# Performance work log

Hardware: AMD Instinct MI355X
Metric: run time of the kernel (lower is better)

Reference implementation:

```python
import jax, jax.numpy as jnp
import numpy as np

N = 100000
IN_CH = 128
HID = 128
H = HID // 2  # per-sign half width = 64
E = 1200000
L = 3  # num_layers


def _mean_agg(x, src, dst, n):
    # mean of x[src] scattered to dst (source_to_target message passing)
    s = jax.ops.segment_sum(x[src], dst, num_segments=n)
    cnt = jax.ops.segment_sum(jnp.ones(src.shape[0], x.dtype), dst, num_segments=n)
    return s / jnp.maximum(cnt, 1.0)[:, None]


def setup_inputs() -> dict:
    key = jax.random.key(0)
    ks = jax.random.split(key, 16)
    sc = 0.05
    inp = {
        "x": jax.random.normal(ks[0], (N, IN_CH), jnp.float32),
        "pos_edge_index": jax.random.randint(ks[1], (2, E), 0, N, jnp.int64),
        "neg_edge_index": jax.random.randint(ks[2], (2, E), 0, N, jnp.int64),
        # conv1 (first_aggr=True): per-sign Linear on aggregated + on root
        "Wp_l": jax.random.normal(ks[3], (IN_CH, H), jnp.float32) * sc,
        "Wp_r": jax.random.normal(ks[4], (IN_CH, H), jnp.float32) * sc,
        "bp": jnp.zeros((H,), jnp.float32),
        "Wn_l": jax.random.normal(ks[5], (IN_CH, H), jnp.float32) * sc,
        "Wn_r": jax.random.normal(ks[6], (IN_CH, H), jnp.float32) * sc,
        "bn": jnp.zeros((H,), jnp.float32),
        # convs (first_aggr=False), stacked over L-1 layers
        "Wl_pos": jax.random.normal(ks[7], (L - 1, 2 * H, H), jnp.float32) * sc,
        "Wr_pos": jax.random.normal(ks[8], (L - 1, H, H), jnp.float32) * sc,
        "b_pos": jnp.zeros((L - 1, H), jnp.float32),
        "Wl_neg": jax.random.normal(ks[9], (L - 1, 2 * H, H), jnp.float32) * sc,
        "Wr_neg": jax.random.normal(ks[10], (L - 1, H, H), jnp.float32) * sc,
        "b_neg": jnp.zeros((L - 1, H), jnp.float32),
    }
    return inp


def reference(x, pos_edge_index, neg_edge_index,
              Wp_l, Wp_r, bp, Wn_l, Wn_r, bn,
              Wl_pos, Wr_pos, b_pos, Wl_neg, Wr_neg, b_neg):
    n = x.shape[0]
    ps, pd = pos_edge_index[0], pos_edge_index[1]
    ns, nd = neg_edge_index[0], neg_edge_index[1]

    # ---- conv1, first_aggr=True ----
    agg_p = _mean_agg(x, ps, pd, n)   # [N, IN_CH]
    agg_n = _mean_agg(x, ns, nd, n)
    out_pos = agg_p @ Wp_l + x @ Wp_r + bp   # [N, H]
    out_neg = agg_n @ Wn_l + x @ Wn_r + bn
    z = jnp.tanh(jnp.concatenate([out_pos, out_neg], axis=1))  # [N, 2H]

    # ---- convs, first_aggr=False ----
    for l in range(Wl_pos.shape[0]):
        x_p, x_n = z[:, :H], z[:, H:]
        ap_p = _mean_agg(x_p, ps, pd, n)   # pos-agg of pos half
        an_n = _mean_agg(x_n, ns, nd, n)   # neg-agg of neg half
        ap_n = _mean_agg(x_n, ps, pd, n)   # pos-agg of neg half
        an_p = _mean_agg(x_p, ns, nd, n)   # neg-agg of pos half
        o_p = (jnp.concatenate([ap_p, an_n], axis=1) @ Wl_pos[l]
               + x_p @ Wr_pos[l] + b_pos[l])
        o_n = (jnp.concatenate([ap_n, an_p], axis=1) @ Wl_neg[l]
               + x_n @ Wr_neg[l] + b_neg[l])
        z = jnp.tanh(jnp.concatenate([o_p, o_n], axis=1))
    return z  # [N, HID]
```

## Files before the change

kernel.cpp:

```cpp
#include <hip/hip_runtime.h>
#include <math.h>

#define CH 128
#define BSHIFT 9
#define BNODES (1 << BSHIFT)
#define CHUNKE 16384

typedef __attribute__((ext_vector_type(8))) short bf16x8;
typedef __attribute__((ext_vector_type(4))) float f32x4;

__global__ __launch_bounds__(256) void hist_kernel(const int* __restrict__ pe,
                                                   const int* __restrict__ ne,
                                                   int* __restrict__ hb,
                                                   int NBr, int G, int M, int E) {
    const int g = blockIdx.x, s = blockIdx.y, t = threadIdx.x;
    const int* __restrict__ dst = (s ? ne : pe) + E;
    __shared__ int h[512];
    for (int i = t; i < NBr; i += 256) h[i] = 0;
    __syncthreads();
    const int e0 = g * CHUNKE, e1 = min(e0 + CHUNKE, E);
    for (int e = e0 + t; e < e1; e += 256) atomicAdd(&h[dst[e] >> BSHIFT], 1);
    __syncthreads();
    int* out = hb + (size_t)s * M;
    for (int b = t; b < NBr; b += 256) out[b * G + g] = h[b];
}

__global__ __launch_bounds__(1024) void hscan_kernel(int* __restrict__ hb, int M) {
    const int s = blockIdx.y, t = threadIdx.x;
    int* H = hb + (size_t)s * M;
    const int K = (M + 1023) >> 10;
    const int i0 = t * K, i1 = min(i0 + K, M);
    int sum = 0;
    for (int i = i0; i < i1; ++i) sum += H[i];
    __shared__ int sh[1024];
    sh[t] = sum;
    __syncthreads();
    for (int off = 1; off < 1024; off <<= 1) {
        int v = (t >= off) ? sh[t - off] : 0;
        __syncthreads();
        sh[t] += v;
        __syncthreads();
    }
    int run = sh[t] - sum;
    for (int i = i0; i < i1; ++i) { int v = H[i]; H[i] = run; run += v; }
}

__global__ __launch_bounds__(256) void scatter_kernel(const int* __restrict__ pe,
                                                      const int* __restrict__ ne,
                                                      const int* __restrict__ hb,
                                                      int* __restrict__ tmp,
                                                      int NBr, int G, int M, int E) {
    const int g = blockIdx.x, s = blockIdx.y, t = threadIdx.x;
    const int* __restrict__ ed = s ? ne : pe;
    const int* off = hb + (size_t)s * M;
    __shared__ int cur[512];
    for (int b = t; b < NBr; b += 256) cur[b] = off[b * G + g];
    __syncthreads();
    int* out = tmp + (size_t)s * E;
    const int e0 = g * CHUNKE, e1 = min(e0 + CHUNKE, E);
    for (int e = e0 + t; e < e1; e += 256) {
        const int src = ed[e], d = ed[E + e];
        const int p = atomicAdd(&cur[d >> BSHIFT], 1);
        out[p] = (src << BSHIFT) | (d & (BNODES - 1));
    }
}

__global__ __launch_bounds__(256) void bucket_kernel(const int* __restrict__ tmp,
                                                     const int* __restrict__ hb,
                                                     int* __restrict__ row_p,
                                                     int* __restrict__ row_n,
                                                     int* __restrict__ csr_p,
                                                     int* __restrict__ csr_n,
                                                     int NBr, int G, int M, int E, int nN) {
    const int b = blockIdx.x, s = blockIdx.y, t = threadIdx.x;
    const int* off = hb + (size_t)s * M;
    const int lo = off[b * G];
    const int hi = (b + 1 < NBr) ? off[(b + 1) * G] : E;
    const int base = b << BSHIFT;
    const int nloc = min(BNODES, nN - base);
    const int* __restrict__ in = tmp + (size_t)s * E;
    int* __restrict__ row = s ? row_n : row_p;
    int* __restrict__ csr = s ? csr_n : csr_p;
    __shared__ int cnt[BNODES];
    __shared__ int psum[256];
    for (int i = t; i < BNODES; i += 256) cnt[i] = 0;
    __syncthreads();
    for (int e = lo + t; e < hi; e += 256) atomicAdd(&cnt[in[e] & (BNODES - 1)], 1);
    __syncthreads();
    const int c0 = cnt[2 * t], c1 = cnt[2 * t + 1];
    const int ps = c0 + c1;
    psum[t] = ps;
    __syncthreads();
    for (int o = 1; o < 256; o <<= 1) {
        int v = (t >= o) ? psum[t - o] : 0;
        __syncthreads();
        psum[t] += v;
        __syncthreads();
    }
    const int ex = psum[t] - ps;
    cnt[2 * t]     = lo + ex;
    cnt[2 * t + 1] = lo + ex + c0;
    if (2 * t < nloc)     row[base + 2 * t] = lo + ex;
    if (2 * t + 1 < nloc) row[base + 2 * t + 1] = lo + ex + c0;
    if (b == NBr - 1 && t == 0) row[nN] = E;
    __syncthreads();
    for (int e = lo + t; e < hi; e += 256) {
        const int v = in[e];
        const int p = atomicAdd(&cnt[v & (BNODES - 1)], 1);
        csr[p] = (v >> BSHIFT) << 8;
    }
}

__device__ __forceinline__ float fast_tanh(float x) {
    float e = __expf(2.0f * x);
    return 1.0f - 2.0f * __builtin_amdgcn_rcpf(e + 1.0f);
}

__device__ __forceinline__ unsigned short f2bf(float f) {
    unsigned u = __float_as_uint(f);
    u += 0x7fffu + ((u >> 16) & 1u);
    return (unsigned short)(u >> 16);
}

__device__ __forceinline__ float bf_lo(unsigned v) { return __uint_as_float(v << 16); }
__device__ __forceinline__ float bf_hi(unsigned v) { return __uint_as_float(v & 0xffff0000u); }

__global__ __launch_bounds__(256) void cvt_kernel(const float* __restrict__ x,
                                                  unsigned short* __restrict__ xb,
                                                  int total8) {
    const int i = blockIdx.x * 256 + threadIdx.x;
    if (i >= total8) return;
    const float4 u0 = ((const float4*)x)[2 * i];
    const float4 u1 = ((const float4*)x)[2 * i + 1];
    union { bf16x8 v; unsigned short u[8]; } o;
    o.u[0] = f2bf(u0.x); o.u[1] = f2bf(u0.y); o.u[2] = f2bf(u0.z); o.u[3] = f2bf(u0.w);
    o.u[4] = f2bf(u1.x); o.u[5] = f2bf(u1.y); o.u[6] = f2bf(u1.z); o.u[7] = f2bf(u1.w);
    ((bf16x8*)xb)[i] = o.v;
}

#define P1(csr, e, A0, A1, A2, A3) { \
    const int o0 = csr[e], o1 = csr[e + 1]; \
    const uint2 w = *(const uint2*)(fB + (half ? o1 : o0) + off8); \
    A0 += bf_lo(w.x); A1 += bf_hi(w.x); A2 += bf_lo(w.y); A3 += bf_hi(w.y); }

#define T1(csr, e, A0, A1, A2, A3) { \
    if (half == 0) { \
        const uint2 w = *(const uint2*)(fB + csr[e] + off8); \
        A0 += bf_lo(w.x); A1 += bf_hi(w.x); A2 += bf_lo(w.y); A3 += bf_hi(w.y); } }

__global__ __launch_bounds__(256) void agg_kernel(
    const unsigned short* __restrict__ feat,
    unsigned* __restrict__ aggp, unsigned* __restrict__ aggn,
    const int* __restrict__ row_p, const int* __restrict__ csr_p,
    const int* __restrict__ row_n, const int* __restrict__ csr_n, int nN) {
    const int t = threadIdx.x;
    const int wave = t >> 6;
    const int lane = t & 63;
    const int node = blockIdx.x * 4 + wave;
    if (node >= nN) return;
    const char* __restrict__ fB = (const char*)feat;
    const int half = lane >> 5;
    const int off8 = (lane & 31) * 8;
    int ep = __builtin_amdgcn_readfirstlane(row_p[node]);
    const int e1p = __builtin_amdgcn_readfirstlane(row_p[node + 1]);
    int en = __builtin_amdgcn_readfirstlane(row_n[node]);
    const int e1n = __builtin_amdgcn_readfirstlane(row_n[node + 1]);
    const int degp = e1p - ep;
    const int degn = e1n - en;
    float p0 = 0.f, p1 = 0.f, p2 = 0.f, p3 = 0.f;
    float n0 = 0.f, n1 = 0.f, n2 = 0.f, n3 = 0.f;
    while (ep + 8 <= e1p && en + 8 <= e1n) {
        P1(csr_p, ep,     p0, p1, p2, p3);
        P1(csr_p, ep + 2, p0, p1, p2, p3);
        P1(csr_p, ep + 4, p0, p1, p2, p3);
        P1(csr_p, ep + 6, p0, p1, p2, p3);
        P1(csr_n, en,     n0, n1, n2, n3);
        P1(csr_n, en + 2, n0, n1, n2, n3);
        P1(csr_n, en + 4, n0, n1, n2, n3);
        P1(csr_n, en + 6, n0, n1, n2, n3);
        ep += 8; en += 8;
    }
    while (ep + 2 <= e1p && en + 2 <= e1n) {
        P1(csr_p, ep, p0, p1, p2, p3);
        P1(csr_n, en, n0, n1, n2, n3);
        ep += 2; en += 2;
    }
    for (; ep + 1 < e1p; ep += 2) P1(csr_p, ep, p0, p1, p2, p3);
    if (ep < e1p) T1(csr_p, ep, p0, p1, p2, p3);
    for (; en + 1 < e1n; en += 2) P1(csr_n, en, n0, n1, n2, n3);
    if (en < e1n) T1(csr_n, en, n0, n1, n2, n3);

    p0 += __shfl_xor(p0, 32); p1 += __shfl_xor(p1, 32);
    p2 += __shfl_xor(p2, 32); p3 += __shfl_xor(p3, 32);
    n0 += __shfl_xor(n0, 32); n1 += __shfl_xor(n1, 32);
    n2 += __shfl_xor(n2, 32); n3 += __shfl_xor(n3, 32);

    const float invp = 1.0f / (float)(degp > 1 ? degp : 1);
    const float invn = 1.0f / (float)(degn > 1 ? degn : 1);
    const int li = lane & 31;
    if (half == 0) {
        uint2 o;
        o.x = (unsigned)f2bf(p0 * invp) | ((unsigned)f2bf(p1 * invp) << 16);
        o.y = (unsigned)f2bf(p2 * invp) | ((unsigned)f2bf(p3 * invp) << 16);
        ((uint2*)(aggp + (size_t)node * 64))[li] = o;
    } else {
        uint2 o;
        o.x = (unsigned)f2bf(n0 * invn) | ((unsigned)f2bf(n1 * invn) << 16);
        o.y = (unsigned)f2bf(n2 * invn) | ((unsigned)f2bf(n3 * invn) << 16);
        ((uint2*)(aggn + (size_t)node * 64))[li] = o;
    }
}

__global__ __launch_bounds__(64) void wpack_kernel(
    const float* __restrict__ Wp_l, const float* __restrict__ Wp_r,
    const float* __restrict__ Wn_l, const float* __restrict__ Wn_r,
    const float* __restrict__ Wl_pos, const float* __restrict__ Wr_pos,
    const float* __restrict__ Wl_neg, const float* __restrict__ Wr_neg,
    unsigned short* __restrict__ Wpk) {
    const int b = blockIdx.x;
    const int L = b / 96;
    const int rem = b % 96;
    const int ks = rem / 8, nt = rem % 8;
    const int lane = threadIdx.x;
    const int kb = ks * 32 + (lane >> 4) * 8;
    const int n = nt * 16 + (lane & 15);
    unsigned short v[8];
#pragma unroll
    for (int j = 0; j < 8; ++j) {
        const int k = kb + j;
        float w = 0.f;
        if (L == 0) {
            if (k < 128)      w = (n < 64) ? Wp_l[k * 64 + n] : 0.f;
            else if (k < 256) w = (n < 64) ? 0.f : Wn_l[(k - 128) * 64 + (n - 64)];
            else              w = (n < 64) ? Wp_r[(k - 256) * 64 + n]
                                           : Wn_r[(k - 256) * 64 + (n - 64)];
        } else {
            const float* WLp = Wl_pos + (size_t)(L - 1) * 128 * 64;
            const float* WLn = Wl_neg + (size_t)(L - 1) * 128 * 64;
            const float* WRp = Wr_pos + (size_t)(L - 1) * 64 * 64;
            const float* WRn = Wr_neg + (size_t)(L - 1) * 64 * 64;
            if (k < 64)       w = (n < 64) ? WLp[k * 64 + n] : 0.f;
            else if (k < 128) w = (n < 64) ? 0.f : WLn[(k - 64) * 64 + (n - 64)];
            else if (k < 192) w = (n < 64) ? 0.f : WLn[(64 + k - 128) * 64 + (n - 64)];
            else if (k < 256) w = (n < 64) ? WLp[(64 + k - 192) * 64 + n] : 0.f;
            else if (k < 320) w = (n < 64) ? WRp[(k - 256) * 64 + n] : 0.f;
            else              w = (n < 64) ? 0.f : WRn[(k - 320) * 64 + (n - 64)];
        }
        v[j] = f2bf(w);
    }
    unsigned short* dst = Wpk + (size_t)b * 512 + lane * 8;
#pragma unroll
    for (int j = 0; j < 8; ++j) dst[j] = v[j];
}

__global__ void bcat_kernel(const float* __restrict__ bp, const float* __restrict__ bn,
                            const float* __restrict__ b_pos, const float* __restrict__ b_neg,
                            float* __restrict__ bcat) {
    int t = threadIdx.x;
    int L = t >> 7, n = t & 127;
    float v;
    if (L == 0) v = (n < 64) ? bp[n] : bn[n - 64];
    else        v = (n < 64) ? b_pos[(L - 1) * 64 + n] : b_neg[(L - 1) * 64 + (n - 64)];
    bcat[t] = v;
}

template <bool OUTF32>
__global__ __launch_bounds__(256) void gemm_kernel(
    const unsigned short* __restrict__ aggp, const unsigned short* __restrict__ aggn,
    const unsigned short* __restrict__ feat, const unsigned short* __restrict__ Wpk,
    const float* __restrict__ bcat, void* __restrict__ outv, int nN) {
    const int t = threadIdx.x;
    const int wave = __builtin_amdgcn_readfirstlane(t >> 6);
    const int lane = t & 63;
    const int r0 = blockIdx.x * 64 + wave * 16;
    int rowA = r0 + (lane & 15);
    if (rowA >= nN) rowA = nN - 1;
    const int koff = (lane >> 4) * 8;

    __shared__ unsigned short wlds[48 * 512];

    f32x4 acc[8];
#pragma unroll
    for (int i = 0; i < 8; ++i) acc[i] = (f32x4){0.f, 0.f, 0.f, 0.f};

    for (int h = 0; h < 2; ++h) {
        {
            const bf16x8* __restrict__ src = (const bf16x8*)(Wpk + (size_t)(h * 48) * 512);
            bf16x8* dst = (bf16x8*)wlds;
#pragma unroll
            for (int j = 0; j < 12; ++j) dst[t + j * 256] = src[t + j * 256];
        }
        __syncthreads();
#pragma unroll
        for (int ksl = 0; ksl < 6; ++ksl) {
            const int ks = h * 6 + ksl;
            const int kcol = (ks & 3) * 32 + koff;
            const unsigned short* ap = (ks < 4) ? aggp : (ks < 8) ? aggn : feat;
            const bf16x8 a = *(const bf16x8*)(ap + (size_t)rowA * CH + kcol);
            const unsigned short* wl = wlds + (size_t)(ksl * 8) * 512 + lane * 8;
#pragma unroll
            for (int nt = 0; nt < 8; ++nt) {
                const bf16x8 bfr = *(const bf16x8*)(wl + nt * 512);
                acc[nt] = __builtin_amdgcn_mfma_f32_16x16x32_bf16(a, bfr, acc[nt], 0, 0, 0);
            }
        }
        __syncthreads();
    }

    const int col0 = lane & 15;
    const int rq = (lane >> 4) * 4;
#pragma unroll
    for (int nt = 0; nt < 8; ++nt) {
        const int col = nt * 16 + col0;
        const float bias = bcat[col];
#pragma unroll
        for (int r = 0; r < 4; ++r) {
            const int row = r0 + rq + r;
            if (row < nN) {
                const float v = fast_tanh(acc[nt][r] + bias);
                if (OUTF32) ((float*)outv)[(size_t)row * CH + col] = v;
                else ((unsigned short*)outv)[(size_t)row * CH + col] = f2bf(v);
            }
        }
    }
}

extern "C" void kernel_launch(void* const* d_in, const int* in_sizes, int n_in,
                              void* d_out, int out_size, void* d_ws, size_t ws_size,
                              hipStream_t stream) {
    const float* x      = (const float*)d_in[0];
    const int*   pe     = (const int*)d_in[1];
    const int*   ne     = (const int*)d_in[2];
    const float* Wp_l   = (const float*)d_in[3];
    const float* Wp_r   = (const float*)d_in[4];
    const float* bp     = (const float*)d_in[5];
    const float* Wn_l   = (const float*)d_in[6];
    const float* Wn_r   = (const float*)d_in[7];
    const float* bn     = (const float*)d_in[8];
    const float* Wl_pos = (const float*)d_in[9];
    const float* Wr_pos = (const float*)d_in[10];
    const float* b_pos  = (const float*)d_in[11];
    const float* Wl_neg = (const float*)d_in[12];
    const float* Wr_neg = (const float*)d_in[13];
    const float* b_neg  = (const float*)d_in[14];

    const int E = in_sizes[1] / 2;
    const int n = in_sizes[0] / CH;

    const int NBr = (n + BNODES - 1) >> BSHIFT;
    const int G   = (E + CHUNKE - 1) / CHUNKE;
    const int M   = NBr * G;

    unsigned short* A    = (unsigned short*)d_ws;
    unsigned short* B    = A + (size_t)n * CH;
    unsigned short* C    = B + (size_t)n * CH;
    unsigned short* Wpk  = C + (size_t)n * CH;
    float* bcat  = (float*)(Wpk + 147456);
    int* row_p   = (int*)(bcat + 384);
    int* row_n   = row_p + n + 1;
    int* csr_p   = row_n + n + 1;
    int* csr_n   = csr_p + E;
    int* hb      = csr_n + E;
    int* tmp     = (int*)C;
    unsigned short* xb = C;

    hist_kernel<<<dim3(G, 2), 256, 0, stream>>>(pe, ne, hb, NBr, G, M, E);
    wpack_kernel<<<288, 64, 0, stream>>>(Wp_l, Wp_r, Wn_l, Wn_r,
                                         Wl_pos, Wr_pos, Wl_neg, Wr_neg, Wpk);
    bcat_kernel<<<1, 384, 0, stream>>>(bp, bn, b_pos, b_neg, bcat);
    hscan_kernel<<<dim3(1, 2), 1024, 0, stream>>>(hb, M);
    scatter_kernel<<<dim3(G, 2), 256, 0, stream>>>(pe, ne, hb, tmp, NBr, G, M, E);
    bucket_kernel<<<dim3(NBr, 2), 256, 0, stream>>>(tmp, hb, row_p, row_n,
                                                    csr_p, csr_n, NBr, G, M, E, n);
    const int total8 = n * CH / 8;
    cvt_kernel<<<(total8 + 255) / 256, 256, 0, stream>>>(x, xb, total8);

    const dim3 agrid((n + 3) / 4), ablock(256);
    const dim3 ggrid((n + 63) / 64), gblock(256);

    agg_kernel<<<agrid, ablock, 0, stream>>>(
        xb, (unsigned*)A, (unsigned*)B, row_p, csr_p, row_n, csr_n, n);
    gemm_kernel<false><<<ggrid, gblock, 0, stream>>>(
        A, B, xb, Wpk, bcat, A, n);
    agg_kernel<<<agrid, ablock, 0, stream>>>(
        A, (unsigned*)B, (unsigned*)C, row_p, csr_p, row_n, csr_n, n);
    gemm_kernel<false><<<ggrid, gblock, 0, stream>>>(
        B, C, A, Wpk + 96 * 512, bcat + 128, B, n);
    agg_kernel<<<agrid, ablock, 0, stream>>>(
        B, (unsigned*)A, (unsigned*)C, row_p, csr_p, row_n, csr_n, n);
    gemm_kernel<true><<<ggrid, gblock, 0, stream>>>(
        A, C, B, Wpk + 2 * 96 * 512, bcat + 256, d_out, n);
}
```

Measured before the change: 597.5 us.

## Process two row tiles per GEMM wave and fold bias packing into weight pack

```diff
diff --git a/kernel.cpp b/kernel.cpp
--- a/kernel.cpp
+++ b/kernel.cpp
@@ -216,12 +216,24 @@
     const float* __restrict__ Wn_l, const float* __restrict__ Wn_r,
     const float* __restrict__ Wl_pos, const float* __restrict__ Wr_pos,
     const float* __restrict__ Wl_neg, const float* __restrict__ Wr_neg,
-    unsigned short* __restrict__ Wpk) {
+    const float* __restrict__ bp, const float* __restrict__ bn,
+    const float* __restrict__ b_pos, const float* __restrict__ b_neg,
+    unsigned short* __restrict__ Wpk, float* __restrict__ bcat) {
     const int b = blockIdx.x;
+    const int lane = threadIdx.x;
+    if (b == 288) {
+        for (int i = lane; i < 384; i += 64) {
+            int L = i >> 7, n = i & 127;
+            float v;
+            if (L == 0) v = (n < 64) ? bp[n] : bn[n - 64];
+            else        v = (n < 64) ? b_pos[(L - 1) * 64 + n] : b_neg[(L - 1) * 64 + (n - 64)];
+            bcat[i] = v;
+        }
+        return;
+    }
     const int L = b / 96;
     const int rem = b % 96;
     const int ks = rem / 8, nt = rem % 8;
-    const int lane = threadIdx.x;
     const int kb = ks * 32 + (lane >> 4) * 8;
     const int n = nt * 16 + (lane & 15);
     unsigned short v[8];
@@ -253,17 +265,6 @@
     for (int j = 0; j < 8; ++j) dst[j] = v[j];
 }
 
-__global__ void bcat_kernel(const float* __restrict__ bp, const float* __restrict__ bn,
-                            const float* __restrict__ b_pos, const float* __restrict__ b_neg,
-                            float* __restrict__ bcat) {
-    int t = threadIdx.x;
-    int L = t >> 7, n = t & 127;
-    float v;
-    if (L == 0) v = (n < 64) ? bp[n] : bn[n - 64];
-    else        v = (n < 64) ? b_pos[(L - 1) * 64 + n] : b_neg[(L - 1) * 64 + (n - 64)];
-    bcat[t] = v;
-}
-
 template <bool OUTF32>
 __global__ __launch_bounds__(256) void gemm_kernel(
     const unsigned short* __restrict__ aggp, const unsigned short* __restrict__ aggn,
@@ -272,16 +273,21 @@
     const int t = threadIdx.x;
     const int wave = __builtin_amdgcn_readfirstlane(t >> 6);
     const int lane = t & 63;
-    const int r0 = blockIdx.x * 64 + wave * 16;
-    int rowA = r0 + (lane & 15);
-    if (rowA >= nN) rowA = nN - 1;
+    const int r0 = blockIdx.x * 128 + wave * 16;
+    int rowA0 = r0 + (lane & 15);
+    int rowA1 = rowA0 + 64;
+    if (rowA0 >= nN) rowA0 = nN - 1;
+    if (rowA1 >= nN) rowA1 = nN - 1;
     const int koff = (lane >> 4) * 8;
 
     __shared__ unsigned short wlds[48 * 512];
 
-    f32x4 acc[8];
-#pragma unroll
-    for (int i = 0; i < 8; ++i) acc[i] = (f32x4){0.f, 0.f, 0.f, 0.f};
+    f32x4 acc0[8], acc1[8];
+#pragma unroll
+    for (int i = 0; i < 8; ++i) {
+        acc0[i] = (f32x4){0.f, 0.f, 0.f, 0.f};
+        acc1[i] = (f32x4){0.f, 0.f, 0.f, 0.f};
+    }
 
     for (int h = 0; h < 2; ++h) {
         {
@@ -290,18 +296,24 @@
 #pragma unroll
             for (int j = 0; j < 12; ++j) dst[t + j * 256] = src[t + j * 256];
         }
-        __syncthreads();
+        bf16x8 a0[6], a1[6];
 #pragma unroll
         for (int ksl = 0; ksl < 6; ++ksl) {
             const int ks = h * 6 + ksl;
             const int kcol = (ks & 3) * 32 + koff;
             const unsigned short* ap = (ks < 4) ? aggp : (ks < 8) ? aggn : feat;
-            const bf16x8 a = *(const bf16x8*)(ap + (size_t)rowA * CH + kcol);
+            a0[ksl] = *(const bf16x8*)(ap + (size_t)rowA0 * CH + kcol);
+            a1[ksl] = *(const bf16x8*)(ap + (size_t)rowA1 * CH + kcol);
+        }
+        __syncthreads();
+#pragma unroll
+        for (int ksl = 0; ksl < 6; ++ksl) {
             const unsigned short* wl = wlds + (size_t)(ksl * 8) * 512 + lane * 8;
 #pragma unroll
             for (int nt = 0; nt < 8; ++nt) {
                 const bf16x8 bfr = *(const bf16x8*)(wl + nt * 512);
-                acc[nt] = __builtin_amdgcn_mfma_f32_16x16x32_bf16(a, bfr, acc[nt], 0, 0, 0);
+                acc0[nt] = __builtin_amdgcn_mfma_f32_16x16x32_bf16(a0[ksl], bfr, acc0[nt], 0, 0, 0);
+                acc1[nt] = __builtin_amdgcn_mfma_f32_16x16x32_bf16(a1[ksl], bfr, acc1[nt], 0, 0, 0);
             }
         }
         __syncthreads();
@@ -315,11 +327,17 @@
         const float bias = bcat[col];
 #pragma unroll
         for (int r = 0; r < 4; ++r) {
-            const int row = r0 + rq + r;
-            if (row < nN) {
-                const float v = fast_tanh(acc[nt][r] + bias);
-                if (OUTF32) ((float*)outv)[(size_t)row * CH + col] = v;
-                else ((unsigned short*)outv)[(size_t)row * CH + col] = f2bf(v);
+            const int row0 = r0 + rq + r;
+            if (row0 < nN) {
+                const float v = fast_tanh(acc0[nt][r] + bias);
+                if (OUTF32) ((float*)outv)[(size_t)row0 * CH + col] = v;
+                else ((unsigned short*)outv)[(size_t)row0 * CH + col] = f2bf(v);
+            }
+            const int row1 = row0 + 64;
+            if (row1 < nN) {
+                const float v = fast_tanh(acc1[nt][r] + bias);
+                if (OUTF32) ((float*)outv)[(size_t)row1 * CH + col] = v;
+                else ((unsigned short*)outv)[(size_t)row1 * CH + col] = f2bf(v);
             }
         }
     }
@@ -365,9 +383,9 @@
     unsigned short* xb = C;
 
     hist_kernel<<<dim3(G, 2), 256, 0, stream>>>(pe, ne, hb, NBr, G, M, E);
-    wpack_kernel<<<288, 64, 0, stream>>>(Wp_l, Wp_r, Wn_l, Wn_r,
-                                         Wl_pos, Wr_pos, Wl_neg, Wr_neg, Wpk);
-    bcat_kernel<<<1, 384, 0, stream>>>(bp, bn, b_pos, b_neg, bcat);
+    wpack_kernel<<<289, 64, 0, stream>>>(Wp_l, Wp_r, Wn_l, Wn_r,
+                                         Wl_pos, Wr_pos, Wl_neg, Wr_neg,
+                                         bp, bn, b_pos, b_neg, Wpk, bcat);
     hscan_kernel<<<dim3(1, 2), 1024, 0, stream>>>(hb, M);
     scatter_kernel<<<dim3(G, 2), 256, 0, stream>>>(pe, ne, hb, tmp, NBr, G, M, E);
     bucket_kernel<<<dim3(NBr, 2), 256, 0, stream>>>(tmp, hb, row_p, row_n,
@@ -376,7 +394,7 @@
     cvt_kernel<<<(total8 + 255) / 256, 256, 0, stream>>>(x, xb, total8);
 
     const dim3 agrid((n + 3) / 4), ablock(256);
-    const dim3 ggrid((n + 63) / 64), gblock(256);
+    const dim3 ggrid((n + 127) / 128), gblock(256);
 
     agg_kernel<<<agrid, ablock, 0, stream>>>(
         xb, (unsigned*)A, (unsigned*)B, row_p, csr_p, row_n, csr_n, n);
```

After: 608.5 us. No clear change (+1.8%).
